# Performance work log

Measured on AMD Instinct MI355X. Metric: run time of the kernel, lower is better.

## Reference

```python
import jax, jax.numpy as jnp
import numpy as np

N_ATOMS = 100000
N_EDGES = 800000
ATOM_FDIM = 133
HIDDEN = 256
DEPTH = 3
NUM_MOLS = 4096
BN_EPS = 1e-5


def setup_inputs() -> dict:
    key = jax.random.key(0)
    ks = jax.random.split(key, 16)
    f_atoms = jax.random.normal(ks[0], (N_ATOMS, ATOM_FDIM), dtype=jnp.float32)
    edge_index = jax.random.randint(ks[1], (2, N_EDGES), 0, N_ATOMS, dtype=jnp.int64)
    segment_ids = jnp.sort(jax.random.randint(ks[2], (N_ATOMS,), 0, NUM_MOLS, dtype=jnp.int64))
    s = 1.0 / np.sqrt(HIDDEN)
    return {
        "f_atoms": f_atoms,
        "W_in_w": jax.random.normal(ks[3], (ATOM_FDIM, HIDDEN), dtype=jnp.float32) / np.sqrt(ATOM_FDIM),
        "W_in_b": jnp.zeros((HIDDEN,), dtype=jnp.float32),
        "w1": jax.random.normal(ks[4], (DEPTH, HIDDEN, HIDDEN), dtype=jnp.float32) * s,
        "b1": jnp.zeros((DEPTH, HIDDEN), dtype=jnp.float32),
        "g1": jnp.ones((DEPTH, HIDDEN), dtype=jnp.float32),
        "be1": jnp.zeros((DEPTH, HIDDEN), dtype=jnp.float32),
        "w2": jax.random.normal(ks[5], (DEPTH, HIDDEN, HIDDEN), dtype=jnp.float32) * s,
        "b2": jnp.zeros((DEPTH, HIDDEN), dtype=jnp.float32),
        "g2": jnp.ones((DEPTH, HIDDEN), dtype=jnp.float32),
        "be2": jnp.zeros((DEPTH, HIDDEN), dtype=jnp.float32),
        "eps": jnp.zeros((DEPTH,), dtype=jnp.float32),
        "edge_index": edge_index,
        "segment_ids": segment_ids,
    }


def batchnorm(h, gamma, beta):
    # BatchNorm1d with batch statistics over the node dimension (training-mode math)
    mean = jnp.mean(h, axis=0)
    var = jnp.var(h, axis=0)
    return (h - mean) * jax.lax.rsqrt(var + BN_EPS) * gamma + beta


def reference(f_atoms, W_in_w, W_in_b, w1, b1, g1, be1, w2, b2, g2, be2, eps,
              edge_index, segment_ids):
    src, dst = edge_index[0], edge_index[1]
    x = jax.nn.relu(f_atoms @ W_in_w + W_in_b)  # [N, H]
    for i in range(DEPTH):
        agg = jnp.zeros_like(x).at[dst].add(x[src])  # gather + scatter-add
        h = agg + (1.0 + eps[i]) * x                 # epsilon self-term
        h = jax.nn.relu(batchnorm(h @ w1[i] + b1[i], g1[i], be1[i]))
        h = jax.nn.relu(batchnorm(h @ w2[i] + b2[i], g2[i], be2[i]))
        x = h  # dropout = identity (eval)
    sums = jax.ops.segment_sum(x, segment_ids, num_segments=NUM_MOLS)
    counts = jax.ops.segment_sum(jnp.ones((x.shape[0],), x.dtype), segment_ids,
                                 num_segments=NUM_MOLS)
    return sums / jnp.maximum(counts, 1.0)[:, None]  # per-molecule mean
```

## Files before the change

### kernel.cpp

```cpp
#include <hip/hip_runtime.h>
#include <hip/hip_bf16.h>

#define NA 100000
#define NE 800000
#define FDIM 133
#define KIN 192
#define H 256
#define NMOL 4096

typedef __attribute__((ext_vector_type(8))) short s16x8;
typedef __attribute__((ext_vector_type(4))) float f32x4;
typedef __attribute__((ext_vector_type(4))) unsigned int u32x4;

__device__ __forceinline__ float bf2f(unsigned short h) {
    unsigned u = ((unsigned)h) << 16;
    return __builtin_bit_cast(float, u);
}
__device__ __forceinline__ unsigned short f2bf(float f) {
    unsigned u = __builtin_bit_cast(unsigned, f);
    u = u + 0x7FFFu + ((u >> 16) & 1u);
    return (unsigned short)(u >> 16);
}
__device__ __forceinline__ void nt_store16(s16x8 v, void* p) {
    __builtin_nontemporal_store(__builtin_bit_cast(u32x4, v), (u32x4*)p);
}
__device__ __forceinline__ s16x8 nt_load16(const void* p) {
    return __builtin_bit_cast(s16x8, __builtin_nontemporal_load((const u32x4*)p));
}

__device__ __forceinline__ int swz(int row, int g) {
    return row * 64 + ((g ^ (row & 7)) << 3);
}

template<bool A_F32, bool AFFINE, bool RELU_OUT, bool STATS, bool NTA>
__global__ __launch_bounds__(512, 4) void gemm_k(
    const void* __restrict__ Avoid,
    const unsigned short* __restrict__ BT,
    const float* __restrict__ bias,
    const float* __restrict__ aSc, const float* __restrict__ aSh,
    unsigned short* __restrict__ C,
    float* __restrict__ stSum, float* __restrict__ stSq,
    int M, int Kpad)
{
    __shared__ short lsAB[(128 + 256) * 64];
    __shared__ float lsSc[256], lsSh[256];
    __shared__ float lsS[256], lsQ[256];
    short* lsA = lsAB;
    short* lsB = lsAB + 128 * 64;

    const int t = threadIdx.x;
    const int m0 = blockIdx.x * 128;

    if (STATS && t < 256) { lsS[t] = 0.f; lsQ[t] = 0.f; }
    if (AFFINE && t < 256) { lsSc[t] = aSc[t]; lsSh[t] = aSh[t]; }
    if (AFFINE) __syncthreads();

    const int lane = t & 63;
    const int wid = t >> 6;
    const int wm = wid >> 2, wn = wid & 3;
    const int fr = lane & 15, fg = lane >> 4;
    const int srow = t >> 3;
    const int sg = t & 7;

    f32x4 acc[4][4];
    #pragma unroll
    for (int i = 0; i < 4; i++)
        #pragma unroll
        for (int j = 0; j < 4; j++)
            acc[i][j] = f32x4{0.f, 0.f, 0.f, 0.f};

    const int nK = Kpad >> 6;
    s16x8 ra[2], rb[4];

    auto loadRegs = [&](int kc) {
        const int k0 = kc * 64;
        #pragma unroll
        for (int p = 0; p < 2; ++p) {
            int r = srow + p * 64;
            int ga = m0 + r;
            if (A_F32) {
                const float* Af = (const float*)Avoid;
                s16x8 v;
                #pragma unroll
                for (int e = 0; e < 8; ++e) {
                    int k = k0 + sg * 8 + e;
                    float f = (ga < M && k < FDIM) ? Af[(size_t)ga * FDIM + k] : 0.f;
                    v[e] = (short)f2bf(f);
                }
                ra[p] = v;
            } else {
                const unsigned short* A = (const unsigned short*)Avoid;
                s16x8 z = {0,0,0,0,0,0,0,0};
                const void* ap = A + (size_t)ga * Kpad + k0 + sg * 8;
                ra[p] = (ga < M) ? (NTA ? nt_load16(ap) : *(const s16x8*)ap) : z;
            }
        }
        #pragma unroll
        for (int p = 0; p < 4; ++p)
            rb[p] = *(const s16x8*)(BT + (size_t)(srow + p * 64) * Kpad + k0 + sg * 8);
    };
    auto writeLds = [&](int kc) {
        const int k0 = kc * 64;
        #pragma unroll
        for (int p = 0; p < 2; ++p) {
            s16x8 va = ra[p];
            if (AFFINE) {
                #pragma unroll
                for (int e = 0; e < 8; ++e) {
                    int k = k0 + sg * 8 + e;
                    float f = bf2f((unsigned short)va[e]);
                    f = fmaxf(f * lsSc[k] + lsSh[k], 0.f);
                    va[e] = (short)f2bf(f);
                }
            }
            *(s16x8*)&lsA[swz(srow + p * 64, sg)] = va;
        }
        #pragma unroll
        for (int p = 0; p < 4; ++p)
            *(s16x8*)&lsB[swz(srow + p * 64, sg)] = rb[p];
    };

    loadRegs(0);
    for (int kc = 0; kc < nK; ++kc) {
        writeLds(kc);
        __syncthreads();
        if (kc + 1 < nK) loadRegs(kc + 1);
        #pragma unroll
        for (int ks = 0; ks < 2; ++ks) {
            s16x8 af[4], bg[4];
            #pragma unroll
            for (int mi = 0; mi < 4; ++mi)
                af[mi] = *(const s16x8*)&lsA[swz(wm * 64 + mi * 16 + fr, ks * 4 + fg)];
            #pragma unroll
            for (int ni = 0; ni < 4; ++ni)
                bg[ni] = *(const s16x8*)&lsB[swz(wn * 64 + ni * 16 + fr, ks * 4 + fg)];
            #pragma unroll
            for (int mi = 0; mi < 4; ++mi)
                #pragma unroll
                for (int ni = 0; ni < 4; ++ni)
                    acc[mi][ni] = __builtin_amdgcn_mfma_f32_16x16x32_bf16(
                        af[mi], bg[ni], acc[mi][ni], 0, 0, 0);
        }
        __syncthreads();
    }

    const int CST = 264;
    #pragma unroll
    for (int hm = 0; hm < 2; ++hm) {
        __syncthreads();
        if (wm == hm) {
            #pragma unroll
            for (int ni = 0; ni < 4; ++ni) {
                int lcol = wn * 64 + ni * 16 + fr;
                float bc = bias[lcol];
                float cs = 0.f, cq = 0.f;
                #pragma unroll
                for (int mi = 0; mi < 4; ++mi) {
                    #pragma unroll
                    for (int r = 0; r < 4; ++r) {
                        int rl = mi * 16 + fg * 4 + r;
                        float v = acc[mi][ni][r] + bc;
                        if (RELU_OUT) v = fmaxf(v, 0.f);
                        if (STATS && (m0 + hm * 64 + rl < M)) { cs += v; cq += v * v; }
                        lsAB[rl * CST + lcol] = (short)f2bf(v);
                    }
                }
                if (STATS) {
                    atomicAdd(&lsS[lcol], cs);
                    atomicAdd(&lsQ[lcol], cq);
                }
            }
        }
        __syncthreads();
        #pragma unroll
        for (int p = 0; p < 4; ++p) {
            int idx = p * 512 + t;
            int rl = idx >> 5;
            int col = (idx & 31) * 8;
            int row = m0 + hm * 64 + rl;
            if (row < M)
                nt_store16(*(const s16x8*)&lsAB[rl * CST + col], C + (size_t)row * H + col);
        }
    }

    if (STATS) {
        __syncthreads();
        if (t < 256) {
            atomicAdd(&stSum[t], lsS[t]);
            atomicAdd(&stSq[t], lsQ[t]);
        }
    }
}

__global__ void bnfin_k(float* __restrict__ sum, float* __restrict__ sumsq,
                        const float* __restrict__ g, const float* __restrict__ be,
                        float* __restrict__ scOut, float* __restrict__ shOut) {
    int c = threadIdx.x;
    float mean = sum[c] * (1.0f / NA);
    float var = sumsq[c] * (1.0f / NA) - mean * mean;
    float sc = g[c] * rsqrtf(var + 1e-5f);
    scOut[c] = sc;
    shOut[c] = be[c] - mean * sc;
    sum[c] = 0.f; sumsq[c] = 0.f;
}

__global__ void zero_k(int* __restrict__ counts, float* __restrict__ st, int* __restrict__ rowstart) {
    int i = blockIdx.x * 256 + threadIdx.x;
    if (i < NA) counts[i] = 0;
    if (blockIdx.x == 0) {
        st[threadIdx.x] = 0.f; st[threadIdx.x + 256] = 0.f;
        if (threadIdx.x == 0) rowstart[NA] = NE;
    }
}

__global__ void hist_k(const int* __restrict__ dst, int* __restrict__ counts) {
    int e = blockIdx.x * 256 + threadIdx.x;
    if (e < NE) atomicAdd(&counts[dst[e]], 1);
}
__global__ void scan1_k(const int* __restrict__ counts, int* __restrict__ excl, int* __restrict__ bsum) {
    __shared__ int sd[256];
    int i = blockIdx.x * 256 + threadIdx.x;
    int c = (i < NA) ? counts[i] : 0;
    sd[threadIdx.x] = c;
    __syncthreads();
    for (int off = 1; off < 256; off <<= 1) {
        int v = (threadIdx.x >= off) ? sd[threadIdx.x - off] : 0;
        __syncthreads();
        sd[threadIdx.x] += v;
        __syncthreads();
    }
    if (i < NA) excl[i] = sd[threadIdx.x] - c;
    if (threadIdx.x == 255) bsum[blockIdx.x] = sd[255];
}
__global__ void scan2_k(int* __restrict__ bsum, int nb) {
    __shared__ int sd[512];
    int t = threadIdx.x;
    int v = (t < nb) ? bsum[t] : 0;
    sd[t] = v;
    __syncthreads();
    for (int off = 1; off < 512; off <<= 1) {
        int u = (t >= off) ? sd[t - off] : 0;
        __syncthreads();
        sd[t] += u;
        __syncthreads();
    }
    if (t < nb) bsum[t] = sd[t] - v;
}
__global__ void scan3_k(int* __restrict__ rowstart, const int* __restrict__ bsum, int* __restrict__ cursor) {
    int i = blockIdx.x * 256 + threadIdx.x;
    if (i < NA) {
        int v = rowstart[i] + bsum[blockIdx.x];
        rowstart[i] = v;
        cursor[i] = v;
    }
}
__global__ void fill_k(const int* __restrict__ src, const int* __restrict__ dstArr,
                       int* __restrict__ cursor, int* __restrict__ esrc) {
    int e = blockIdx.x * 256 + threadIdx.x;
    if (e < NE) {
        int d = dstArr[e];
        int pos = atomicAdd(&cursor[d], 1);
        esrc[pos] = src[e];
    }
}

template<bool AFF>
__global__ __launch_bounds__(256) void agg_k(const unsigned short* __restrict__ X,
    const float* __restrict__ sc, const float* __restrict__ sh,
    const int* __restrict__ rowstart,
    const int* __restrict__ esrc, const float* __restrict__ epsArr, int layer,
    unsigned short* __restrict__ AGG)
{
    int wid = threadIdx.x >> 6, lane = threadIdx.x & 63;
    int row = blockIdx.x * 4 + wid;
    int half = lane >> 5;
    int c0 = (lane & 31) * 8;

    float s8[8], h8[8];
    if (AFF) {
        f32x4 a = *(const f32x4*)(sc + c0), b = *(const f32x4*)(sc + c0 + 4);
        f32x4 c = *(const f32x4*)(sh + c0), d = *(const f32x4*)(sh + c0 + 4);
        #pragma unroll
        for (int e = 0; e < 4; e++) { s8[e] = a[e]; s8[e + 4] = b[e]; h8[e] = c[e]; h8[e + 4] = d[e]; }
    }

    float a0[8] = {0,0,0,0,0,0,0,0}, a1[8] = {0,0,0,0,0,0,0,0};
    auto addv = [&](s16x8 u, float* a) {
        #pragma unroll
        for (int e = 0; e < 8; e++) {
            float f = bf2f((unsigned short)u[e]);
            if (AFF) f = fmaxf(f * s8[e] + h8[e], 0.f);
            a[e] += f;
        }
    };

    int s = rowstart[row], eEnd = rowstart[row + 1];
    int cnt = eEnd - s, mid = s + (cnt >> 1);
    int i = half ? mid : s;
    int end = half ? eEnd : mid;
    for (; i + 3 < end; i += 4) {
        int e0 = esrc[i], e1 = esrc[i + 1], e2 = esrc[i + 2], e3 = esrc[i + 3];
        s16x8 u0 = *(const s16x8*)(X + (size_t)e0 * H + c0);
        s16x8 u1 = *(const s16x8*)(X + (size_t)e1 * H + c0);
        s16x8 u2 = *(const s16x8*)(X + (size_t)e2 * H + c0);
        s16x8 u3 = *(const s16x8*)(X + (size_t)e3 * H + c0);
        addv(u0, a0); addv(u1, a1); addv(u2, a0); addv(u3, a1);
    }
    for (; i < end; ++i) {
        int e0 = esrc[i];
        s16x8 u = *(const s16x8*)(X + (size_t)e0 * H + c0);
        addv(u, a0);
    }

    if (half == 0) {
        float e1 = 1.0f + epsArr[layer];
        s16x8 u = *(const s16x8*)(X + (size_t)row * H + c0);
        #pragma unroll
        for (int e = 0; e < 8; e++) {
            float f = bf2f((unsigned short)u[e]);
            if (AFF) f = fmaxf(f * s8[e] + h8[e], 0.f);
            a0[e] += f * e1;
        }
    }

    s16x8 o;
    #pragma unroll
    for (int e = 0; e < 8; e++) {
        float tot = a0[e] + a1[e];
        tot += __shfl_xor(tot, 32);
        o[e] = (short)f2bf(tot);
    }
    if (half == 0)
        nt_store16(o, AGG + (size_t)row * H + c0);
}

__global__ void prep_all_k(const float* __restrict__ Win, const float* __restrict__ w1,
                           const float* __restrict__ w2, unsigned short* __restrict__ BTall) {
    int i = blockIdx.x * 256 + threadIdx.x;
    const int NIN = 256 * KIN;
    if (i < NIN) {
        int n = i / KIN, k = i % KIN;
        BTall[i] = (k < FDIM) ? f2bf(Win[(size_t)k * 256 + n]) : (unsigned short)0;
    } else if (i < NIN + 6 * 65536) {
        int j = i - NIN;
        int d = j >> 16, r = j & 65535;
        int n = r >> 8, k = r & 255;
        const float* W = (d & 1) ? w2 : w1;
        BTall[i] = f2bf(W[(size_t)(d >> 1) * 65536 + (size_t)k * 256 + n]);
    }
}

__global__ void molstart_k(const int* __restrict__ seg, int* __restrict__ ms) {
    int m = blockIdx.x * 256 + threadIdx.x;
    if (m <= NMOL) {
        int lo = 0, hi = NA;
        while (lo < hi) { int mid = (lo + hi) >> 1; if (seg[mid] < m) lo = mid + 1; else hi = mid; }
        ms[m] = lo;
    }
}
__global__ __launch_bounds__(64) void mean_k(const unsigned short* __restrict__ X,
    const float* __restrict__ sc, const float* __restrict__ sh,
    const int* __restrict__ ms, float* __restrict__ out)
{
    int m = blockIdx.x, lane = threadIdx.x;
    int half = lane >> 5;
    int c0 = (lane & 31) * 8;
    float s8[8], h8[8];
    {
        f32x4 a = *(const f32x4*)(sc + c0), b = *(const f32x4*)(sc + c0 + 4);
        f32x4 c = *(const f32x4*)(sh + c0), d = *(const f32x4*)(sh + c0 + 4);
        #pragma unroll
        for (int e = 0; e < 4; e++) { s8[e] = a[e]; s8[e + 4] = b[e]; h8[e] = c[e]; h8[e + 4] = d[e]; }
    }
    int a = ms[m], b = ms[m + 1];
    float acc[8] = {0,0,0,0,0,0,0,0};
    for (int r = a + half; r < b; r += 2) {
        s16x8 u = *(const s16x8*)(X + (size_t)r * H + c0);
        #pragma unroll
        for (int e = 0; e < 8; e++)
            acc[e] += fmaxf(bf2f((unsigned short)u[e]) * s8[e] + h8[e], 0.f);
    }
    float inv = (b > a) ? 1.0f / (float)(b - a) : 0.0f;
    f32x4 o0, o1;
    #pragma unroll
    for (int e = 0; e < 8; e++) {
        float tot = acc[e] + __shfl_xor(acc[e], 32);
        tot *= inv;
        if (e < 4) o0[e] = tot; else o1[e - 4] = tot;
    }
    if (half == 0) {
        *(f32x4*)(out + (size_t)m * H + c0) = o0;
        *(f32x4*)(out + (size_t)m * H + c0 + 4) = o1;
    }
}

extern "C" void kernel_launch(void* const* d_in, const int* in_sizes, int n_in,
                              void* d_out, int out_size, void* d_ws, size_t ws_size,
                              hipStream_t stream) {
    const float* f_atoms = (const float*)d_in[0];
    const float* W_in_w  = (const float*)d_in[1];
    const float* W_in_b  = (const float*)d_in[2];
    const float* w1  = (const float*)d_in[3];
    const float* b1  = (const float*)d_in[4];
    const float* g1  = (const float*)d_in[5];
    const float* be1 = (const float*)d_in[6];
    const float* w2  = (const float*)d_in[7];
    const float* b2  = (const float*)d_in[8];
    const float* g2  = (const float*)d_in[9];
    const float* be2 = (const float*)d_in[10];
    const float* epsArr = (const float*)d_in[11];
    const int* edge = (const int*)d_in[12];
    const int* seg  = (const int*)d_in[13];
    float* out = (float*)d_out;

    char* w = (char*)d_ws;
    size_t off = 0;
    auto alloc = [&](size_t bytes) {
        char* p = w + off;
        off = (off + bytes + 255) & ~(size_t)255;
        return p;
    };
    unsigned short* X   = (unsigned short*)alloc((size_t)NA * H * 2);
    unsigned short* AGG = (unsigned short*)alloc((size_t)NA * H * 2);
    unsigned short* T1  = (unsigned short*)alloc((size_t)NA * H * 2);
    unsigned short* BTall = (unsigned short*)alloc(((size_t)256 * KIN + 6 * 65536) * 2);
    float* stSum = (float*)alloc(256 * 4);
    float* stSq  = (float*)alloc(256 * 4);
    float* sc1 = (float*)alloc(256 * 4);
    float* sh1 = (float*)alloc(256 * 4);
    float* sc2 = (float*)alloc(256 * 4);
    float* sh2 = (float*)alloc(256 * 4);
    int* counts   = (int*)alloc((size_t)NA * 4);
    int* rowstart = (int*)alloc((size_t)(NA + 1) * 4);
    int* cursor   = (int*)alloc((size_t)NA * 4);
    int* esrc     = (int*)alloc((size_t)NE * 4);
    int* bsum     = (int*)alloc(512 * 4);
    int* ms       = (int*)alloc((NMOL + 1) * 4);

    unsigned short* BTin = BTall;
    unsigned short* BT1[3], *BT2[3];
    for (int d = 0; d < 3; ++d) {
        BT1[d] = BTall + 256 * KIN + (size_t)(2 * d) * 65536;
        BT2[d] = BTall + 256 * KIN + (size_t)(2 * d + 1) * 65536;
    }

    const int* esrcIn = edge;
    const int* edst   = edge + NE;

    zero_k<<<(NA + 255) / 256, 256, 0, stream>>>(counts, stSum, rowstart);
    prep_all_k<<<(256 * KIN + 6 * 65536 + 255) / 256, 256, 0, stream>>>(W_in_w, w1, w2, BTall);

    hist_k<<<(NE + 255) / 256, 256, 0, stream>>>(edst, counts);
    scan1_k<<<391, 256, 0, stream>>>(counts, rowstart, bsum);
    scan2_k<<<1, 512, 0, stream>>>(bsum, 391);
    scan3_k<<<391, 256, 0, stream>>>(rowstart, bsum, cursor);
    fill_k<<<(NE + 255) / 256, 256, 0, stream>>>(esrcIn, edst, cursor, esrc);
    molstart_k<<<(NMOL + 256) / 256, 256, 0, stream>>>(seg, ms);

    const int GB = (NA + 127) / 128;

    gemm_k<true, false, true, false, false><<<GB, 512, 0, stream>>>(
        f_atoms, BTin, W_in_b, nullptr, nullptr, X, nullptr, nullptr, NA, KIN);

    for (int d = 0; d < 3; ++d) {
        if (d == 0)
            agg_k<false><<<NA / 4, 256, 0, stream>>>(X, nullptr, nullptr,
                rowstart, esrc, epsArr, d, AGG);
        else
            agg_k<true><<<NA / 4, 256, 0, stream>>>(X, sc2, sh2,
                rowstart, esrc, epsArr, d, AGG);
        gemm_k<false, false, false, true, true><<<GB, 512, 0, stream>>>(
            AGG, BT1[d], b1 + d * 256, nullptr, nullptr, T1, stSum, stSq, NA, 256);
        bnfin_k<<<1, 256, 0, stream>>>(stSum, stSq, g1 + d * 256, be1 + d * 256, sc1, sh1);
        gemm_k<false, true, false, true, true><<<GB, 512, 0, stream>>>(
            T1, BT2[d], b2 + d * 256, sc1, sh1, X, stSum, stSq, NA, 256);
        bnfin_k<<<1, 256, 0, stream>>>(stSum, stSq, g2 + d * 256, be2 + d * 256, sc2, sh2);
    }

    mean_k<<<NMOL, 64, 0, stream>>>(X, sc2, sh2, ms, out);
}
```

Before: 884.2 us.

## Halve GEMM M-tile to 64 rows and shrink LDS for higher occupancy

The GEMM block tile drops from 128 to 64 rows, so each wave holds a 2x4 accumulator tile instead of 4x4. LDS is reduced by dropping the scale/shift and stats arrays and reusing the A/B buffers for stats and output staging. The launch bound goes to 8 blocks per CU, and the BN affine parameters are now read straight from global memory as vectors. The goal is more resident waves to hide latency, at the cost of reloading the full B tile for twice as many blocks and twice as many global stats atomics.

New measurement: 1.796 ms. +103.1%, slower.

```diff
diff --git a/kernel.cpp b/kernel.cpp
--- a/kernel.cpp
+++ b/kernel.cpp
@@ -33,7 +33,7 @@
 }
 
 template<bool A_F32, bool AFFINE, bool RELU_OUT, bool STATS, bool NTA>
-__global__ __launch_bounds__(512, 4) void gemm_k(
+__global__ __launch_bounds__(512, 8) void gemm_k(
     const void* __restrict__ Avoid,
     const unsigned short* __restrict__ BT,
     const float* __restrict__ bias,
@@ -42,18 +42,11 @@
     float* __restrict__ stSum, float* __restrict__ stSq,
     int M, int Kpad)
 {
-    __shared__ short lsAB[(128 + 256) * 64];
-    __shared__ float lsSc[256], lsSh[256];
-    __shared__ float lsS[256], lsQ[256];
-    short* lsA = lsAB;
-    short* lsB = lsAB + 128 * 64;
+    __shared__ short lsA[64 * 64];
+    __shared__ short lsB[256 * 64];
 
     const int t = threadIdx.x;
-    const int m0 = blockIdx.x * 128;
-
-    if (STATS && t < 256) { lsS[t] = 0.f; lsQ[t] = 0.f; }
-    if (AFFINE && t < 256) { lsSc[t] = aSc[t]; lsSh[t] = aSh[t]; }
-    if (AFFINE) __syncthreads();
+    const int m0 = blockIdx.x * 64;
 
     const int lane = t & 63;
     const int wid = t >> 6;
@@ -62,38 +55,34 @@
     const int srow = t >> 3;
     const int sg = t & 7;
 
-    f32x4 acc[4][4];
+    f32x4 acc[2][4];
     #pragma unroll
-    for (int i = 0; i < 4; i++)
+    for (int i = 0; i < 2; i++)
         #pragma unroll
         for (int j = 0; j < 4; j++)
             acc[i][j] = f32x4{0.f, 0.f, 0.f, 0.f};
 
     const int nK = Kpad >> 6;
-    s16x8 ra[2], rb[4];
+    s16x8 ra, rb[4];
 
     auto loadRegs = [&](int kc) {
         const int k0 = kc * 64;
-        #pragma unroll
-        for (int p = 0; p < 2; ++p) {
-            int r = srow + p * 64;
-            int ga = m0 + r;
-            if (A_F32) {
-                const float* Af = (const float*)Avoid;
-                s16x8 v;
-                #pragma unroll
-                for (int e = 0; e < 8; ++e) {
-                    int k = k0 + sg * 8 + e;
-                    float f = (ga < M && k < FDIM) ? Af[(size_t)ga * FDIM + k] : 0.f;
-                    v[e] = (short)f2bf(f);
-                }
-                ra[p] = v;
-            } else {
-                const unsigned short* A = (const unsigned short*)Avoid;
-                s16x8 z = {0,0,0,0,0,0,0,0};
-                const void* ap = A + (size_t)ga * Kpad + k0 + sg * 8;
-                ra[p] = (ga < M) ? (NTA ? nt_load16(ap) : *(const s16x8*)ap) : z;
+        int ga = m0 + srow;
+        if (A_F32) {
+            const float* Af = (const float*)Avoid;
+            s16x8 v;
+            #pragma unroll
+            for (int e = 0; e < 8; ++e) {
+                int k = k0 + sg * 8 + e;
+                float f = (ga < M && k < FDIM) ? Af[(size_t)ga * FDIM + k] : 0.f;
+                v[e] = (short)f2bf(f);
             }
+            ra = v;
+        } else {
+            const unsigned short* A = (const unsigned short*)Avoid;
+            s16x8 z = {0,0,0,0,0,0,0,0};
+            const void* ap = A + (size_t)ga * Kpad + k0 + sg * 8;
+            ra = (ga < M) ? (NTA ? nt_load16(ap) : *(const s16x8*)ap) : z;
         }
         #pragma unroll
         for (int p = 0; p < 4; ++p)
@@ -101,20 +90,21 @@
     };
     auto writeLds = [&](int kc) {
         const int k0 = kc * 64;
-        #pragma unroll
-        for (int p = 0; p < 2; ++p) {
-            s16x8 va = ra[p];
-            if (AFFINE) {
-                #pragma unroll
-                for (int e = 0; e < 8; ++e) {
-                    int k = k0 + sg * 8 + e;
-                    float f = bf2f((unsigned short)va[e]);
-                    f = fmaxf(f * lsSc[k] + lsSh[k], 0.f);
-                    va[e] = (short)f2bf(f);
-                }
+        s16x8 va = ra;
+        if (AFFINE) {
+            f32x4 s0 = *(const f32x4*)&aSc[k0 + sg * 8];
+            f32x4 s1 = *(const f32x4*)&aSc[k0 + sg * 8 + 4];
+            f32x4 h0 = *(const f32x4*)&aSh[k0 + sg * 8];
+            f32x4 h1 = *(const f32x4*)&aSh[k0 + sg * 8 + 4];
+            #pragma unroll
+            for (int e = 0; e < 4; ++e) {
+                float f0 = fmaxf(bf2f((unsigned short)va[e]) * s0[e] + h0[e], 0.f);
+                float f1 = fmaxf(bf2f((unsigned short)va[e + 4]) * s1[e] + h1[e], 0.f);
+                va[e] = (short)f2bf(f0);
+                va[e + 4] = (short)f2bf(f1);
             }
-            *(s16x8*)&lsA[swz(srow + p * 64, sg)] = va;
-        }
+        }
+        *(s16x8*)&lsA[swz(srow, sg)] = va;
         #pragma unroll
         for (int p = 0; p < 4; ++p)
             *(s16x8*)&lsB[swz(srow + p * 64, sg)] = rb[p];
@@ -127,15 +117,15 @@
         if (kc + 1 < nK) loadRegs(kc + 1);
         #pragma unroll
         for (int ks = 0; ks < 2; ++ks) {
-            s16x8 af[4], bg[4];
-            #pragma unroll
-            for (int mi = 0; mi < 4; ++mi)
-                af[mi] = *(const s16x8*)&lsA[swz(wm * 64 + mi * 16 + fr, ks * 4 + fg)];
+            s16x8 af[2], bg[4];
+            #pragma unroll
+            for (int mi = 0; mi < 2; ++mi)
+                af[mi] = *(const s16x8*)&lsA[swz(wm * 32 + mi * 16 + fr, ks * 4 + fg)];
             #pragma unroll
             for (int ni = 0; ni < 4; ++ni)
                 bg[ni] = *(const s16x8*)&lsB[swz(wn * 64 + ni * 16 + fr, ks * 4 + fg)];
             #pragma unroll
-            for (int mi = 0; mi < 4; ++mi)
+            for (int mi = 0; mi < 2; ++mi)
                 #pragma unroll
                 for (int ni = 0; ni < 4; ++ni)
                     acc[mi][ni] = __builtin_amdgcn_mfma_f32_16x16x32_bf16(
@@ -144,7 +134,12 @@
         __syncthreads();
     }
 
+    float* lsS = (float*)&lsA[0];
+    float* lsQ = lsS + 256;
+    short* cst = &lsB[0];
     const int CST = 264;
+    if (STATS && t < 256) { lsS[t] = 0.f; lsQ[t] = 0.f; }
+
     #pragma unroll
     for (int hm = 0; hm < 2; ++hm) {
         __syncthreads();
@@ -155,14 +150,14 @@
                 float bc = bias[lcol];
                 float cs = 0.f, cq = 0.f;
                 #pragma unroll
-                for (int mi = 0; mi < 4; ++mi) {
+                for (int mi = 0; mi < 2; ++mi) {
                     #pragma unroll
                     for (int r = 0; r < 4; ++r) {
                         int rl = mi * 16 + fg * 4 + r;
                         float v = acc[mi][ni][r] + bc;
                         if (RELU_OUT) v = fmaxf(v, 0.f);
-                        if (STATS && (m0 + hm * 64 + rl < M)) { cs += v; cq += v * v; }
-                        lsAB[rl * CST + lcol] = (short)f2bf(v);
+                        if (STATS && (m0 + hm * 32 + rl < M)) { cs += v; cq += v * v; }
+                        cst[rl * CST + lcol] = (short)f2bf(v);
                     }
                 }
                 if (STATS) {
@@ -173,22 +168,19 @@
         }
         __syncthreads();
         #pragma unroll
-        for (int p = 0; p < 4; ++p) {
+        for (int p = 0; p < 2; ++p) {
             int idx = p * 512 + t;
             int rl = idx >> 5;
             int col = (idx & 31) * 8;
-            int row = m0 + hm * 64 + rl;
+            int row = m0 + hm * 32 + rl;
             if (row < M)
-                nt_store16(*(const s16x8*)&lsAB[rl * CST + col], C + (size_t)row * H + col);
-        }
-    }
-
-    if (STATS) {
-        __syncthreads();
-        if (t < 256) {
-            atomicAdd(&stSum[t], lsS[t]);
-            atomicAdd(&stSq[t], lsQ[t]);
-        }
+                nt_store16(*(const s16x8*)&cst[rl * CST + col], C + (size_t)row * H + col);
+        }
+    }
+    __syncthreads();
+    if (STATS && t < 256) {
+        atomicAdd(&stSum[t], lsS[t]);
+        atomicAdd(&stSq[t], lsQ[t]);
     }
 }
 
@@ -457,7 +449,7 @@
     fill_k<<<(NE + 255) / 256, 256, 0, stream>>>(esrcIn, edst, cursor, esrc);
     molstart_k<<<(NMOL + 256) / 256, 256, 0, stream>>>(seg, ms);
 
-    const int GB = (NA + 127) / 128;
+    const int GB = (NA + 63) / 64;
 
     gemm_k<true, false, true, false, false><<<GB, 512, 0, stream>>>(
         f_atoms, BTin, W_in_b, nullptr, nullptr, X, nullptr, nullptr, NA, KIN);
```
